# Performance work log

Measured on AMD Instinct MI355X. Metric: run time of the kernel, lower is better.

The kernel has to match this reference:

```python
import jax, jax.numpy as jnp
import numpy as np

B, N, DIM = 256, 196, 384
H, KD, VD = 12, 32, 32
RES = 14
EPS = 1e-5


def _build_bias_idxs():
    pts = [(i, j) for i in range(RES) for j in range(RES)]
    offs, idxs = {}, []
    for p1 in pts:
        for p2 in pts:
            o = (abs(p1[0] - p2[0]), abs(p1[1] - p2[1]))
            if o not in offs:
                offs[o] = len(offs)
            idxs.append(offs[o])
    return jnp.asarray(np.array(idxs, dtype=np.int32).reshape(N, N))


def setup_inputs() -> dict:
    key = jax.random.key(0)
    ks = jax.random.split(key, 4)
    return {
        "x": jax.random.normal(ks[0], (B, N, DIM), dtype=jnp.float32),
        "norm_w": jnp.ones((DIM,), jnp.float32),
        "norm_b": jnp.zeros((DIM,), jnp.float32),
        "qkv_w": jax.random.normal(ks[1], (H * (VD + 2 * KD), DIM), jnp.float32) * 0.02,
        "qkv_b": jnp.zeros((H * (VD + 2 * KD),), jnp.float32),
        "attention_biases": jax.random.normal(ks[2], (H, RES * RES), jnp.float32) * 0.02,
        "proj_w": jax.random.normal(ks[3], (DIM, H * VD), jnp.float32) * 0.02,
        "proj_b": jnp.zeros((DIM,), jnp.float32),
        "bias_idxs": _build_bias_idxs(),
    }


def reference(x, norm_w, norm_b, qkv_w, qkv_b, attention_biases, proj_w, proj_b, bias_idxs):
    scale = KD ** -0.5
    # LayerNorm over feature dim
    mu = jnp.mean(x, axis=-1, keepdims=True)
    var = jnp.mean(jnp.square(x - mu), axis=-1, keepdims=True)
    xn = (x - mu) * jax.lax.rsqrt(var + EPS) * norm_w + norm_b
    # QKV projection: [B,N,H*(2*KD+VD)] -> [B,N,H,*]
    qkv = (jnp.einsum("bnd,fd->bnf", xn, qkv_w) + qkv_b).reshape(B, N, H, 2 * KD + VD)
    q, k, v = qkv[..., :KD], qkv[..., KD:2 * KD], qkv[..., 2 * KD:]
    # Relative-position bias gathered into [H,N,N]
    attn_bias = attention_biases[:, bias_idxs]
    # Scores [B,H,N,N] with bias, softmax, AV
    scores = jnp.einsum("bnhk,bmhk->bhnm", q * scale, k) + attn_bias
    probs = jax.nn.softmax(scores, axis=-1)
    out = jnp.einsum("bhnm,bmhv->bnhv", probs, v).reshape(B, N, H * VD)
    return jnp.einsum("bnf,df->bnd", out, proj_w) + proj_b
```

## Files before the change

kernel.cpp:

```cpp
#include <hip/hip_runtime.h>

#define B_    256
#define N_    196
#define NP_   208
#define VSTR_ 264
#define DIM_  384
#define H_    12
#define KD_   32
#define VD_   32
#define F_    1152
#define ROWS_ (B_ * N_)
#define SCALE_ 0.17677669529663687f
#define EPS_  1e-5f

typedef __bf16 bf16_t;
typedef __bf16 bf16x2 __attribute__((ext_vector_type(2)));
typedef __bf16 bf16x4 __attribute__((ext_vector_type(4)));
typedef __bf16 bf16x8 __attribute__((ext_vector_type(8)));
typedef float  f32x4  __attribute__((ext_vector_type(4)));

__device__ __forceinline__ f32x4 mfma16(bf16x8 a, bf16x8 b, f32x4 c) {
    return __builtin_amdgcn_mfma_f32_16x16x32_bf16(a, b, c, 0, 0, 0);
}

__device__ __forceinline__ void gl2lds(const bf16_t* g, bf16_t* l) {
    __builtin_amdgcn_global_load_lds(
        (const __attribute__((address_space(1))) void*)g,
        (__attribute__((address_space(3))) void*)l, 16, 0, 0);
}

__global__ __launch_bounds__(256) void cvt_w(const float* __restrict__ src,
                                             bf16_t* __restrict__ dst) {
    const int i = (blockIdx.x * 256 + threadIdx.x) * 4;
    const float4 v = *(const float4*)(src + i);
    bf16x4 o = {(bf16_t)v.x, (bf16_t)v.y, (bf16_t)v.z, (bf16_t)v.w};
    *(bf16x4*)(dst + i) = o;
}

__global__ __launch_bounds__(256) void ln_kernel(const float* __restrict__ x,
                                                 const float* __restrict__ w,
                                                 const float* __restrict__ bvec,
                                                 bf16_t* __restrict__ xn) {
    const int lane = threadIdx.x & 63;
    const int row  = blockIdx.x * 4 + (threadIdx.x >> 6);
    const float* xr = x + (size_t)row * DIM_;
    const float4 a = *(const float4*)(xr + lane * 4);
    const float2 c = *(const float2*)(xr + 256 + lane * 2);
    float s  = a.x + a.y + a.z + a.w + c.x + c.y;
    float s2 = a.x*a.x + a.y*a.y + a.z*a.z + a.w*a.w + c.x*c.x + c.y*c.y;
    #pragma unroll
    for (int o = 32; o > 0; o >>= 1) {
        s  += __shfl_xor(s, o);
        s2 += __shfl_xor(s2, o);
    }
    const float mu = s * (1.f / 384.f);
    const float rs = rsqrtf(s2 * (1.f / 384.f) - mu * mu + EPS_);
    const float4 w4 = *(const float4*)(w + lane * 4);
    const float2 w2 = *(const float2*)(w + 256 + lane * 2);
    const float4 b4 = *(const float4*)(bvec + lane * 4);
    const float2 b2 = *(const float2*)(bvec + 256 + lane * 2);
    bf16_t* orow = xn + (size_t)row * DIM_;
    bf16x4 o4 = {(bf16_t)((a.x - mu) * rs * w4.x + b4.x),
                 (bf16_t)((a.y - mu) * rs * w4.y + b4.y),
                 (bf16_t)((a.z - mu) * rs * w4.z + b4.z),
                 (bf16_t)((a.w - mu) * rs * w4.w + b4.w)};
    *(bf16x4*)(orow + lane * 4) = o4;
    bf16x2 o2 = {(bf16_t)((c.x - mu) * rs * w2.x + b2.x),
                 (bf16_t)((c.y - mu) * rs * w2.y + b2.y)};
    *(bf16x2*)(orow + 256 + lane * 2) = o2;
}

__global__ __launch_bounds__(256) void bias_gather(const float* __restrict__ biases,
                                                   const int* __restrict__ idxs,
                                                   bf16_t* __restrict__ biasT) {
    const int e = blockIdx.x * 256 + threadIdx.x;
    if (e >= H_ * NP_ * NP_) return;
    const int h = e / (NP_ * NP_);
    const int r = e % (NP_ * NP_);
    const int m = r / NP_;
    const int q = r % NP_;
    const float v = (m < N_ && q < N_) ? biases[h * N_ + idxs[q * N_ + m]] : -1e30f;
    biasT[e] = (bf16_t)v;
}

template <typename OutT>
__global__ __launch_bounds__(256) void gemm_mfma(const bf16_t* __restrict__ A,
                                                 const bf16_t* __restrict__ Wt,
                                                 const float* __restrict__ bias,
                                                 OutT* __restrict__ C,
                                                 int M, int Nout, int K) {
    __shared__ __align__(16) bf16_t As[128][32];
    __shared__ __align__(16) bf16_t Bs[128][32];
    const int tid  = threadIdx.x;
    const int lane = tid & 63;
    const int wv   = tid >> 6;
    const int ln   = lane & 15;
    const int ko   = lane >> 4;
    const int wr   = (wv >> 1) * 64;
    const int wc   = (wv & 1) * 64;
    const size_t bm = (size_t)blockIdx.x * 128;
    const size_t bn = (size_t)blockIdx.y * 128;

    const int srow = wv * 16 + (lane >> 2);
    const int scol = (lane & 3) * 8;
    const bf16_t* gA0 = A  + (bm + srow) * K + scol;
    const bf16_t* gA1 = gA0 + (size_t)64 * K;
    const bf16_t* gB0 = Wt + (bn + srow) * K + scol;
    const bf16_t* gB1 = gB0 + (size_t)64 * K;
    bf16_t* lA0 = &As[srow][scol];
    bf16_t* lA1 = &As[srow + 64][scol];
    bf16_t* lB0 = &Bs[srow][scol];
    bf16_t* lB1 = &Bs[srow + 64][scol];

    f32x4 acc[4][4];
    #pragma unroll
    for (int i = 0; i < 4; i++)
        #pragma unroll
        for (int j = 0; j < 4; j++)
            acc[i][j] = (f32x4){0.f, 0.f, 0.f, 0.f};

    for (int k0 = 0; k0 < K; k0 += 32) {
        gl2lds(gA0 + k0, lA0);
        gl2lds(gA1 + k0, lA1);
        gl2lds(gB0 + k0, lB0);
        gl2lds(gB1 + k0, lB1);
        __syncthreads();
        bf16x8 af[4], bfr[4];
        #pragma unroll
        for (int i = 0; i < 4; i++)
            af[i] = *(const bf16x8*)&As[wr + i * 16 + ln][ko * 8];
        #pragma unroll
        for (int j = 0; j < 4; j++)
            bfr[j] = *(const bf16x8*)&Bs[wc + j * 16 + ln][ko * 8];
        #pragma unroll
        for (int i = 0; i < 4; i++)
            #pragma unroll
            for (int j = 0; j < 4; j++)
                acc[i][j] = mfma16(bfr[j], af[i], acc[i][j]);
        __syncthreads();
    }

    #pragma unroll
    for (int j = 0; j < 4; j++) {
        const int jc = wc + j * 16 + ko * 4;
        const float4 b4 = *(const float4*)(bias + bn + jc);
        #pragma unroll
        for (int i = 0; i < 4; i++) {
            const size_t row = bm + wr + i * 16 + ln;
            const float v0 = acc[i][j][0] + b4.x;
            const float v1 = acc[i][j][1] + b4.y;
            const float v2 = acc[i][j][2] + b4.z;
            const float v3 = acc[i][j][3] + b4.w;
            OutT* dst = C + row * (size_t)Nout + bn + jc;
            if constexpr (sizeof(OutT) == 2) {
                bf16x4 o = {(bf16_t)v0, (bf16_t)v1, (bf16_t)v2, (bf16_t)v3};
                *(bf16x4*)dst = o;
            } else {
                float4 o = {v0, v1, v2, v3};
                *(float4*)dst = o;
            }
        }
    }
}

__global__ __launch_bounds__(256) void attn_mfma(const bf16_t* __restrict__ qkv,
                                                 const bf16_t* __restrict__ biasT,
                                                 bf16_t* __restrict__ out) {
    const int b = blockIdx.x / H_;
    const int h = blockIdx.x % H_;
    __shared__ __align__(16) bf16_t Ks[NP_][32];
    __shared__ __align__(16) bf16_t Vt[VD_][VSTR_];
    const int tid  = threadIdx.x;
    const int lane = tid & 63;
    const int wv   = tid >> 6;
    const int ln   = lane & 15;
    const int ko   = lane >> 4;

    {
        const int rsub = lane >> 2;
        const int col  = (lane & 3) * 8;
        for (int c = wv; c < 13; c += 4) {
            const int row  = c * 16 + rsub;
            const int srow = min(row, N_ - 1);
            gl2lds(qkv + ((size_t)(b * N_ + srow) * H_ + h) * 96 + KD_ + col,
                   &Ks[row][col]);
        }
    }
    if (tid < 224) {
        const int m  = tid;
        const int kk = (m & ~31) + ((m & 15) >> 2) * 8 + ((m >> 4) & 1) * 4 + (m & 3);
        const bf16_t* src = qkv + ((size_t)(b * N_ + min(m, N_ - 1)) * H_ + h) * 96 + 2 * KD_;
        #pragma unroll
        for (int c4 = 0; c4 < 4; c4++) {
            bf16x8 v8 = {bf16_t(0), bf16_t(0), bf16_t(0), bf16_t(0),
                         bf16_t(0), bf16_t(0), bf16_t(0), bf16_t(0)};
            if (m < N_) v8 = *(const bf16x8*)(src + c4 * 8);
            #pragma unroll
            for (int j = 0; j < 8; j++) Vt[c4 * 8 + j][kk] = v8[j];
        }
    }
    __syncthreads();

    bf16x8 kf[13];
    #pragma unroll
    for (int c = 0; c < 13; c++)
        kf[c] = *(const bf16x8*)&Ks[c * 16 + ln][ko * 8];

    for (int t = wv; t < 13; t += 4) {
        const int q    = t * 16 + ln;
        const int qrow = min(q, N_ - 1);
        const bf16x8 qf =
            *(const bf16x8*)(qkv + ((size_t)(b * N_ + qrow) * H_ + h) * 96 + ko * 8);

        f32x4 sc[13];
        __builtin_amdgcn_s_setprio(1);
        #pragma unroll
        for (int c = 0; c < 13; c++) {
            f32x4 z = {0.f, 0.f, 0.f, 0.f};
            sc[c] = mfma16(kf[c], qf, z);
        }
        __builtin_amdgcn_s_setprio(0);

        const bf16_t* bT = biasT + ((size_t)(h * NP_) + ko * 4) * NP_ + t * 16 + ln;
        float mx = -1e30f;
        #pragma unroll
        for (int c = 0; c < 13; c++)
            #pragma unroll
            for (int r = 0; r < 4; r++) {
                const float s = sc[c][r] * SCALE_ + (float)bT[(c * 16 + r) * NP_];
                sc[c][r] = s;
                mx = fmaxf(mx, s);
            }
        mx = fmaxf(mx, __shfl_xor(mx, 16));
        mx = fmaxf(mx, __shfl_xor(mx, 32));
        float sum = 0.f;
        #pragma unroll
        for (int c = 0; c < 13; c++)
            #pragma unroll
            for (int r = 0; r < 4; r++) {
                const float p = __expf(sc[c][r] - mx);
                sc[c][r] = p;
                sum += p;
            }
        sum += __shfl_xor(sum, 16);
        sum += __shfl_xor(sum, 32);
        const float inv = 1.f / sum;

        f32x4 o0 = {0.f, 0.f, 0.f, 0.f};
        f32x4 o1 = {0.f, 0.f, 0.f, 0.f};
        __builtin_amdgcn_s_setprio(1);
        #pragma unroll
        for (int g = 0; g < 7; g++) {
            bf16x8 pf;
            #pragma unroll
            for (int jj = 0; jj < 4; jj++) pf[jj] = (bf16_t)sc[2 * g][jj];
            if (g < 6) {
                #pragma unroll
                for (int jj = 0; jj < 4; jj++) pf[4 + jj] = (bf16_t)sc[2 * g + 1][jj];
            } else {
                pf[4] = bf16_t(0); pf[5] = bf16_t(0);
                pf[6] = bf16_t(0); pf[7] = bf16_t(0);
            }
            const bf16x8 v0 = *(const bf16x8*)&Vt[ln][g * 32 + ko * 8];
            const bf16x8 v1 = *(const bf16x8*)&Vt[16 + ln][g * 32 + ko * 8];
            o0 = mfma16(v0, pf, o0);
            o1 = mfma16(v1, pf, o1);
        }
        __builtin_amdgcn_s_setprio(0);

        if (q < N_) {
            bf16_t* dst = out + (size_t)(b * N_ + q) * DIM_ + h * VD_ + ko * 4;
            bf16x4 oa = {(bf16_t)(o0[0] * inv), (bf16_t)(o0[1] * inv),
                         (bf16_t)(o0[2] * inv), (bf16_t)(o0[3] * inv)};
            bf16x4 ob = {(bf16_t)(o1[0] * inv), (bf16_t)(o1[1] * inv),
                         (bf16_t)(o1[2] * inv), (bf16_t)(o1[3] * inv)};
            *(bf16x4*)dst = oa;
            *(bf16x4*)(dst + 16) = ob;
        }
    }
}

extern "C" void kernel_launch(void* const* d_in, const int* in_sizes, int n_in,
                              void* d_out, int out_size, void* d_ws, size_t ws_size,
                              hipStream_t stream) {
    const float* x        = (const float*)d_in[0];
    const float* norm_w   = (const float*)d_in[1];
    const float* norm_b   = (const float*)d_in[2];
    const float* qkv_w    = (const float*)d_in[3];
    const float* qkv_b    = (const float*)d_in[4];
    const float* att_bias = (const float*)d_in[5];
    const float* proj_w   = (const float*)d_in[6];
    const float* proj_b   = (const float*)d_in[7];
    const int*   bias_idx = (const int*)d_in[8];
    float* out = (float*)d_out;

    char* ws = (char*)d_ws;
    size_t off = 0;
    bf16_t* xn       = (bf16_t*)(ws + off); off += (size_t)ROWS_ * DIM_ * 2;
    bf16_t* qkvbuf   = (bf16_t*)(ws + off); off += (size_t)ROWS_ * F_ * 2;
    bf16_t* attn_out = (bf16_t*)(ws + off); off += (size_t)ROWS_ * DIM_ * 2;
    bf16_t* biasT    = (bf16_t*)(ws + off); off += (size_t)H_ * NP_ * NP_ * 2;
    bf16_t* wq_bf    = (bf16_t*)(ws + off); off += (size_t)F_ * DIM_ * 2;
    bf16_t* wp_bf    = (bf16_t*)(ws + off); off += (size_t)DIM_ * DIM_ * 2;

    cvt_w<<<(F_ * DIM_) / 1024, 256, 0, stream>>>(qkv_w, wq_bf);
    cvt_w<<<(DIM_ * DIM_) / 1024, 256, 0, stream>>>(proj_w, wp_bf);
    ln_kernel<<<ROWS_ / 4, 256, 0, stream>>>(x, norm_w, norm_b, xn);
    bias_gather<<<(H_ * NP_ * NP_ + 255) / 256, 256, 0, stream>>>(att_bias, bias_idx, biasT);
    gemm_mfma<bf16_t><<<dim3(ROWS_ / 128, F_ / 128), 256, 0, stream>>>(
        xn, wq_bf, qkv_b, qkvbuf, ROWS_, F_, DIM_);
    attn_mfma<<<B_ * H_, 256, 0, stream>>>(qkvbuf, biasT, attn_out);
    gemm_mfma<float><<<dim3(ROWS_ / 128, DIM_ / 128), 256, 0, stream>>>(
        attn_out, wp_bf, proj_b, out, ROWS_, DIM_, DIM_);
}
```

Baseline: 358.6 us.

## Double-buffer GEMM LDS tiles with K=64, XOR swizzle, and swapped grid order

Rewrites the MFMA GEMM main loop to use two LDS buffers with a 64-wide K tile, so the next tile is prefetched while the current one is computed and only one barrier is needed per iteration. The LDS layout uses an XOR swizzle on 16-byte slots to reduce bank conflicts on the fragment reads. The grid is transposed so that blocks sharing an A row tile run next to each other, which should improve L2 reuse of activations. LDS use grows to 64 KB per block, which may lower occupancy.

```diff
diff --git a/kernel.cpp b/kernel.cpp
--- a/kernel.cpp
+++ b/kernel.cpp
@@ -89,8 +89,8 @@
                                                  const float* __restrict__ bias,
                                                  OutT* __restrict__ C,
                                                  int M, int Nout, int K) {
-    __shared__ __align__(16) bf16_t As[128][32];
-    __shared__ __align__(16) bf16_t Bs[128][32];
+    __shared__ __align__(16) bf16_t As[2][128][64];
+    __shared__ __align__(16) bf16_t Bs[2][128][64];
     const int tid  = threadIdx.x;
     const int lane = tid & 63;
     const int wv   = tid >> 6;
@@ -98,19 +98,15 @@
     const int ko   = lane >> 4;
     const int wr   = (wv >> 1) * 64;
     const int wc   = (wv & 1) * 64;
-    const size_t bm = (size_t)blockIdx.x * 128;
-    const size_t bn = (size_t)blockIdx.y * 128;
-
-    const int srow = wv * 16 + (lane >> 2);
-    const int scol = (lane & 3) * 8;
-    const bf16_t* gA0 = A  + (bm + srow) * K + scol;
-    const bf16_t* gA1 = gA0 + (size_t)64 * K;
-    const bf16_t* gB0 = Wt + (bn + srow) * K + scol;
-    const bf16_t* gB1 = gB0 + (size_t)64 * K;
-    bf16_t* lA0 = &As[srow][scol];
-    bf16_t* lA1 = &As[srow + 64][scol];
-    bf16_t* lB0 = &Bs[srow][scol];
-    bf16_t* lB1 = &Bs[srow + 64][scol];
+    const size_t bm = (size_t)blockIdx.y * 128;
+    const size_t bn = (size_t)blockIdx.x * 128;
+
+    const int grow  = lane >> 3;
+    const int gslot = (lane & 7) ^ grow;
+    const int srow  = wv * 32 + grow;
+    const bf16_t* gA = A  + (bm + srow) * K + gslot * 8;
+    const bf16_t* gB = Wt + (bn + srow) * K + gslot * 8;
+    const int ldst = wv * 4 * 512 + lane * 8;
 
     f32x4 acc[4][4];
     #pragma unroll
@@ -119,25 +115,50 @@
         for (int j = 0; j < 4; j++)
             acc[i][j] = (f32x4){0.f, 0.f, 0.f, 0.f};
 
-    for (int k0 = 0; k0 < K; k0 += 32) {
-        gl2lds(gA0 + k0, lA0);
-        gl2lds(gA1 + k0, lA1);
-        gl2lds(gB0 + k0, lB0);
-        gl2lds(gB1 + k0, lB1);
+    bf16_t* As0 = &As[0][0][0];
+    bf16_t* Bs0 = &Bs[0][0][0];
+
+    #pragma unroll
+    for (int j = 0; j < 4; j++) {
+        gl2lds(gA + (size_t)j * 8 * K, As0 + ldst + j * 512);
+        gl2lds(gB + (size_t)j * 8 * K, Bs0 + ldst + j * 512);
+    }
+    __syncthreads();
+
+    const int ntiles = K >> 6;
+    int cur = 0;
+    for (int t = 0; t < ntiles; ++t) {
+        if (t + 1 < ntiles) {
+            const int k0 = (t + 1) << 6;
+            bf16_t* dA = As0 + (cur ^ 1) * (128 * 64) + ldst;
+            bf16_t* dB = Bs0 + (cur ^ 1) * (128 * 64) + ldst;
+            #pragma unroll
+            for (int j = 0; j < 4; j++) {
+                gl2lds(gA + k0 + (size_t)j * 8 * K, dA + j * 512);
+                gl2lds(gB + k0 + (size_t)j * 8 * K, dB + j * 512);
+            }
+        }
+        #pragma unroll
+        for (int kh = 0; kh < 2; kh++) {
+            bf16x8 af[4], bfr[4];
+            #pragma unroll
+            for (int i = 0; i < 4; i++) {
+                const int row = wr + i * 16 + ln;
+                af[i] = *(const bf16x8*)&As[cur][row][(((kh << 2) | ko) ^ (ln & 7)) * 8];
+            }
+            #pragma unroll
+            for (int j = 0; j < 4; j++) {
+                const int row = wc + j * 16 + ln;
+                bfr[j] = *(const bf16x8*)&Bs[cur][row][(((kh << 2) | ko) ^ (ln & 7)) * 8];
+            }
+            #pragma unroll
+            for (int i = 0; i < 4; i++)
+                #pragma unroll
+                for (int j = 0; j < 4; j++)
+                    acc[i][j] = mfma16(bfr[j], af[i], acc[i][j]);
+        }
         __syncthreads();
-        bf16x8 af[4], bfr[4];
-        #pragma unroll
-        for (int i = 0; i < 4; i++)
-            af[i] = *(const bf16x8*)&As[wr + i * 16 + ln][ko * 8];
-        #pragma unroll
-        for (int j = 0; j < 4; j++)
-            bfr[j] = *(const bf16x8*)&Bs[wc + j * 16 + ln][ko * 8];
-        #pragma unroll
-        for (int i = 0; i < 4; i++)
-            #pragma unroll
-            for (int j = 0; j < 4; j++)
-                acc[i][j] = mfma16(bfr[j], af[i], acc[i][j]);
-        __syncthreads();
+        cur ^= 1;
     }
 
     #pragma unroll
@@ -307,9 +328,9 @@
     cvt_w<<<(DIM_ * DIM_) / 1024, 256, 0, stream>>>(proj_w, wp_bf);
     ln_kernel<<<ROWS_ / 4, 256, 0, stream>>>(x, norm_w, norm_b, xn);
     bias_gather<<<(H_ * NP_ * NP_ + 255) / 256, 256, 0, stream>>>(att_bias, bias_idx, biasT);
-    gemm_mfma<bf16_t><<<dim3(ROWS_ / 128, F_ / 128), 256, 0, stream>>>(
+    gemm_mfma<bf16_t><<<dim3(F_ / 128, ROWS_ / 128), 256, 0, stream>>>(
         xn, wq_bf, qkv_b, qkvbuf, ROWS_, F_, DIM_);
     attn_mfma<<<B_ * H_, 256, 0, stream>>>(qkvbuf, biasT, attn_out);
-    gemm_mfma<float><<<dim3(ROWS_ / 128, DIM_ / 128), 256, 0, stream>>>(
+    gemm_mfma<float><<<dim3(DIM_ / 128, ROWS_ / 128), 256, 0, stream>>>(
         attn_out, wp_bf, proj_b, out, ROWS_, DIM_, DIM_);
 }
```

New measurement: 364.9 us. Within noise of the previous version (+1.7%).
